# Kernel optimization log

Hardware: AMD Instinct MI355X
Metric: run time of the kernel (lower is better)

## Reference

```python
import jax, jax.numpy as jnp
import numpy as np

HEADS = 8
DIM_HEAD = 64


def setup_inputs() -> dict:
    key = jax.random.key(0)
    k1, k2, k3 = jax.random.split(key, 3)
    dim_in = 256
    hidden = HEADS * DIM_HEAD  # 512
    x = jax.random.normal(k1, (2, dim_in, 64, 64), dtype=jnp.float32)
    # 1x1 conv weights stored as [out_ch, in_ch]
    w_qkv = jax.random.normal(k2, (3 * hidden, dim_in), dtype=jnp.float32) * (1.0 / np.sqrt(dim_in))
    w_out = jax.random.normal(k3, (dim_in, hidden), dtype=jnp.float32) * (1.0 / np.sqrt(hidden))
    b_out = jnp.zeros((dim_in,), dtype=jnp.float32)
    return {"x": x, "w_qkv": w_qkv, "w_out": w_out, "b_out": b_out}


def reference(x, w_qkv, w_out, b_out):
    b, c, H, W = x.shape
    S = H * W
    scale = 1.0 / np.sqrt(DIM_HEAD)
    # 1x1 conv == per-pixel linear projection
    qkv = jnp.einsum('bcxy,oc->boxy', x, w_qkv)  # [b, 3*hidden, H, W]
    q, k, v = jnp.split(qkv, 3, axis=1)
    # 'b (h c) x y -> b h c (x y)'
    def to_heads(z):
        return z.reshape(b, HEADS, DIM_HEAD, S)
    q = to_heads(q) * scale
    k = to_heads(k)
    v = to_heads(v)
    sim = jnp.einsum('bhdi,bhdj->bhij', q, k)  # [b, h, S, S]
    sim = sim - jax.lax.stop_gradient(jnp.max(sim, axis=-1, keepdims=True))
    attn = jax.nn.softmax(sim, axis=-1)
    out = jnp.einsum('bhij,bhdj->bhid', attn, v)  # [b, h, S, d]
    # 'b h (x y) d -> b (h d) x y'
    out = out.transpose(0, 1, 3, 2).reshape(b, HEADS * DIM_HEAD, H, W)
    return jnp.einsum('bcxy,oc->boxy', out, w_out) + b_out[None, :, None, None]
```

## Files before the change

### kernel.cpp

```cpp
#include <hip/hip_runtime.h>
#include <cmath>

#define S_TOT 4096
#define CIN   256
#define HID   512
#define NHEAD 8
#define DIMH  64

typedef __attribute__((ext_vector_type(8))) short bf16x8;
typedef __attribute__((ext_vector_type(4))) float f32x4;
typedef __attribute__((ext_vector_type(16))) float f32x16;
typedef __attribute__((address_space(1))) const void gv_t;
typedef __attribute__((address_space(3))) void lv_t;

__device__ __forceinline__ ushort f2bf(float f) {
    union { float f; unsigned u; } v; v.f = f;
    unsigned r = (v.u + 0x7FFFu + ((v.u >> 16) & 1u)) >> 16;
    return (ushort)r;
}

__device__ __forceinline__ float bf2f(ushort u) {
    union { unsigned u; float f; } v; v.u = ((unsigned)u) << 16; return v.f;
}

__device__ __forceinline__ float exp2_fast(float x) {
    float r; asm("v_exp_f32 %0, %1" : "=v"(r) : "v"(x)); return r;
}

__device__ __forceinline__ unsigned cvt_pk_bf16(float lo, float hi) {
    unsigned r; asm("v_cvt_pk_bf16_f32 %0, %1, %2" : "=v"(r) : "v"(lo), "v"(hi)); return r;
}

#define QSCALE 0.18033688011112042f

__global__ __launch_bounds__(256)
void cast_f32_bf16(const float* __restrict__ in, ushort* __restrict__ out, long n) {
    long i = ((long)blockIdx.x * 256 + threadIdx.x) * 4;
    if (i < n) {
        float4 v = *(const float4*)&in[i];
        ushort4 p;
        p.x = f2bf(v.x); p.y = f2bf(v.y); p.z = f2bf(v.z); p.w = f2bf(v.w);
        *(ushort4*)&out[i] = p;
    }
}

__global__ __launch_bounds__(256)
void transpose_cast_x(const float* __restrict__ x, ushort* __restrict__ xt) {
    __shared__ float tb[64][65];
    const int t = threadIdx.x;
    const int s0 = blockIdx.x * 64, c0 = blockIdx.y * 64;
    const long xb = (long)blockIdx.z * CIN * S_TOT;
    #pragma unroll
    for (int i = 0; i < 16; ++i) {
        int idx = t + i * 256;
        int c = idx >> 6, s = idx & 63;
        tb[c][s] = x[xb + (long)(c0 + c) * S_TOT + s0 + s];
    }
    __syncthreads();
    const long ob = (long)blockIdx.z * S_TOT * CIN;
    const int s = t >> 2, cq = (t & 3) * 16;
    #pragma unroll
    for (int j = 0; j < 4; ++j) {
        ushort4 pk;
        pk.x = f2bf(tb[cq + j * 4 + 0][s]);
        pk.y = f2bf(tb[cq + j * 4 + 1][s]);
        pk.z = f2bf(tb[cq + j * 4 + 2][s]);
        pk.w = f2bf(tb[cq + j * 4 + 3][s]);
        *(ushort4*)&xt[ob + (long)(s0 + s) * CIN + c0 + cq + j * 4] = pk;
    }
}

template<int MODE>
__global__ __launch_bounds__(256)
void gemm_mfma_kernel(const ushort* __restrict__ Ag, const ushort* __restrict__ Bg,
                      void* __restrict__ outp, const float* __restrict__ bias,
                      int Kdim, long strideA, long strideB) {
    __shared__ __attribute__((aligned(16))) ushort Abuf[128 * 64];
    __shared__ __attribute__((aligned(16))) ushort Bbuf[128 * 64];
    const int t = threadIdx.x, lane = t & 63;
    const int l15 = lane & 15, g = lane >> 4;
    const int wid = t >> 6, wr = wid >> 1, wc = wid & 1;
    const int bz = blockIdx.z;
    const int am0 = blockIdx.y * 128, bn0 = blockIdx.x * 128;
    Ag += (long)bz * strideA;
    Bg += (long)bz * strideB;

    f32x4 acc[4][4];
    #pragma unroll
    for (int i = 0; i < 4; ++i)
        #pragma unroll
        for (int j = 0; j < 4; ++j)
            acc[i][j] = (f32x4){0.f, 0.f, 0.f, 0.f};

    for (int k0 = 0; k0 < Kdim; k0 += 64) {
        __syncthreads();
        #pragma unroll
        for (int i = 0; i < 4; ++i) {
            const int chunk = t + i * 256;
            const int row = chunk >> 3, sl = chunk & 7;
            const ushort* srcA = Ag + (long)(am0 + row) * Kdim + k0 + ((sl ^ (row & 7)) << 3);
            __builtin_amdgcn_global_load_lds((gv_t*)srcA,
                (lv_t*)((char*)Abuf + (i * 256 + (t & ~63)) * 16), 16, 0, 0);
            const ushort* srcB = Bg + (long)(bn0 + row) * Kdim + k0 + ((sl ^ (row & 7)) << 3);
            __builtin_amdgcn_global_load_lds((gv_t*)srcB,
                (lv_t*)((char*)Bbuf + (i * 256 + (t & ~63)) * 16), 16, 0, 0);
        }
        asm volatile("s_waitcnt vmcnt(0)" ::: "memory");
        __syncthreads();

        bf16x8 bfr[4][2];
        #pragma unroll
        for (int fn = 0; fn < 4; ++fn) {
            const int row = wc * 64 + fn * 16 + l15;
            #pragma unroll
            for (int hf = 0; hf < 2; ++hf)
                bfr[fn][hf] = *(const bf16x8*)((const char*)Bbuf + row * 128
                                + (((hf * 4 + g) ^ (row & 7)) << 4));
        }
        #pragma unroll
        for (int fm = 0; fm < 4; ++fm) {
            const int row = wr * 64 + fm * 16 + l15;
            const bf16x8 a0 = *(const bf16x8*)((const char*)Abuf + row * 128
                                + (((g) ^ (row & 7)) << 4));
            const bf16x8 a1 = *(const bf16x8*)((const char*)Abuf + row * 128
                                + (((4 + g) ^ (row & 7)) << 4));
            #pragma unroll
            for (int fn = 0; fn < 4; ++fn) {
                acc[fm][fn] = __builtin_amdgcn_mfma_f32_16x16x32_bf16(a0, bfr[fn][0], acc[fm][fn], 0, 0, 0);
                acc[fm][fn] = __builtin_amdgcn_mfma_f32_16x16x32_bf16(a1, bfr[fn][1], acc[fm][fn], 0, 0, 0);
            }
        }
    }

    #pragma unroll
    for (int fm = 0; fm < 4; ++fm)
        #pragma unroll
        for (int fn = 0; fn < 4; ++fn)
            #pragma unroll
            for (int r = 0; r < 4; ++r) {
                const int ar = am0 + wr * 64 + fm * 16 + g * 4 + r;
                const int bc = bn0 + wc * 64 + fn * 16 + l15;
                if (MODE == 0) {
                    const int which = bc >> 9, h = (bc >> 6) & 7, d = bc & 63;
                    const float scl = (which == 0) ? QSCALE : 1.0f;
                    ushort* O = (ushort*)outp;
                    O[(long)which * 4194304 + (((long)(bz * NHEAD + h)) * S_TOT + ar) * DIMH + d]
                        = f2bf(acc[fm][fn][r] * scl);
                } else if (MODE == 1) {
                    const int h = ar >> 6, d = ar & 63;
                    const int jm = bc & 15;
                    const int pjm = (jm & 3) | ((jm & 4) << 1) | ((jm & 8) >> 1);
                    const int pc = (bc & ~15) | pjm;
                    ushort* O = (ushort*)outp;
                    O[(((long)(bz * NHEAD + h)) * DIMH + d) * S_TOT + pc] = f2bf(acc[fm][fn][r]);
                } else {
                    float* O = (float*)outp;
                    O[((long)bz * CIN + ar) * S_TOT + bc] = acc[fm][fn][r] + bias[ar];
                }
            }
}

__global__ __launch_bounds__(256, 4)
void attn_mfma_kernel(const ushort* __restrict__ qg, const ushort* __restrict__ kg,
                      const ushort* __restrict__ vg, ushort* __restrict__ pout,
                      float2* __restrict__ mlout) {
    __shared__ __attribute__((aligned(16))) ushort kbuf[2][64 * 64];
    __shared__ __attribute__((aligned(16))) ushort vbuf[2][64 * 64];

    const int t = threadIdx.x;
    const int lane = t & 63, wid = t >> 6;
    const int l31 = lane & 31, h = lane >> 5;
    const int head = blockIdx.y;
    const int b = blockIdx.z >> 1, sp = blockIdx.z & 1;
    const int bh = b * NHEAD + head;
    const int qrow0 = blockIdx.x * 128 + wid * 32;
    const long kbase = (long)sp * (S_TOT / 2);

    const int sw_lo = (l31 ^ (l31 >> 3)) & 7;
    const int sw_hi = sw_lo ^ 4;

    const ushort* qp = qg + ((long)bh * S_TOT + qrow0 + l31) * DIMH + h * 8;
    bf16x8 qfr[4];
    #pragma unroll
    for (int ds = 0; ds < 4; ++ds) qfr[ds] = *(const bf16x8*)(qp + ds * 16);

    f32x16 oacc0 = {}, oacc1 = {};
    f32x16 bias16 = {};
    float nmr = 0.f, lrun = 0.f;

    const long kg_base = (long)bh * S_TOT * DIMH;
    const long vg_base = (long)bh * DIMH * S_TOT;
    const int sl = lane & 7, sr = lane >> 3;

    auto STAGE = [&](int buf, long key0) {
        #pragma unroll
        for (int c = 0; c < 2; ++c) {
            const int row = wid * 16 + c * 8 + sr;
            const int sz = (sl ^ sr ^ (wid * 2 + c)) & 7;
            char* kdst = (char*)(&kbuf[buf][0]) + wid * 2048 + c * 1024;
            char* vdst = (char*)(&vbuf[buf][0]) + wid * 2048 + c * 1024;
            const char* srcK = (const char*)(kg + kg_base + (key0 + row) * DIMH) + (sz << 4);
            __builtin_amdgcn_global_load_lds((gv_t*)srcK, (lv_t*)kdst, 16, 0, 0);
            const char* srcV = (const char*)(vg + vg_base + (long)row * S_TOT + key0) + (sz << 4);
            __builtin_amdgcn_global_load_lds((gv_t*)srcV, (lv_t*)vdst, 16, 0, 0);
        }
    };

    STAGE(0, kbase);
    asm volatile("s_waitcnt vmcnt(0)" ::: "memory");
    __syncthreads();

    const int NT = (S_TOT / 2) / 64;
    for (int kt0 = 0; kt0 < NT; ++kt0) {
        const int cur = kt0 & 1;
        if (kt0 + 1 < NT) STAGE(cur ^ 1, kbase + (long)(kt0 + 1) * 64);

        const char* kb_ = (const char*)(&kbuf[cur][0]);
        const char* vb_ = (const char*)(&vbuf[cur][0]);

        f32x16 s0, s1;
        __builtin_amdgcn_s_setprio(1);
        {
            const bf16x8 kf0 = *(const bf16x8*)(kb_ + l31 * 128 + ((h ^ sw_lo) << 4));
            const bf16x8 kf1 = *(const bf16x8*)(kb_ + 4096 + l31 * 128 + ((h ^ sw_hi) << 4));
            s0 = __builtin_amdgcn_mfma_f32_32x32x16_bf16(kf0, qfr[0], bias16, 0, 0, 0);
            s1 = __builtin_amdgcn_mfma_f32_32x32x16_bf16(kf1, qfr[0], bias16, 0, 0, 0);
        }
        #pragma unroll
        for (int ds = 1; ds < 4; ++ds) {
            const bf16x8 kf0 = *(const bf16x8*)(kb_ + l31 * 128 + (((2 * ds + h) ^ sw_lo) << 4));
            const bf16x8 kf1 = *(const bf16x8*)(kb_ + 4096 + l31 * 128 + (((2 * ds + h) ^ sw_hi) << 4));
            s0 = __builtin_amdgcn_mfma_f32_32x32x16_bf16(kf0, qfr[ds], s0, 0, 0, 0);
            s1 = __builtin_amdgcn_mfma_f32_32x32x16_bf16(kf1, qfr[ds], s1, 0, 0, 0);
        }
        __builtin_amdgcn_s_setprio(0);

        bf16x8 pf0, pf1, pf2, pf3;
        {
            float e[16];
            #pragma unroll
            for (int r = 0; r < 16; ++r) e[r] = exp2_fast(s0[r]);
            #pragma unroll
            for (int r = 0; r < 16; ++r) lrun += e[r];
            union { unsigned u[4]; bf16x8 v; } A_, B_;
            #pragma unroll
            for (int w = 0; w < 4; ++w) A_.u[w] = cvt_pk_bf16(e[2 * w], e[2 * w + 1]);
            #pragma unroll
            for (int w = 0; w < 4; ++w) B_.u[w] = cvt_pk_bf16(e[8 + 2 * w], e[9 + 2 * w]);
            pf0 = A_.v; pf1 = B_.v;
        }
        {
            float e[16];
            #pragma unroll
            for (int r = 0; r < 16; ++r) e[r] = exp2_fast(s1[r]);
            #pragma unroll
            for (int r = 0; r < 16; ++r) lrun += e[r];
            union { unsigned u[4]; bf16x8 v; } A_, B_;
            #pragma unroll
            for (int w = 0; w < 4; ++w) A_.u[w] = cvt_pk_bf16(e[2 * w], e[2 * w + 1]);
            #pragma unroll
            for (int w = 0; w < 4; ++w) B_.u[w] = cvt_pk_bf16(e[8 + 2 * w], e[9 + 2 * w]);
            pf2 = A_.v; pf3 = B_.v;
        }

        __builtin_amdgcn_s_setprio(1);
        {
            const bf16x8 vf00 = *(const bf16x8*)(vb_ + l31 * 128 + ((h ^ sw_lo) << 4));
            const bf16x8 vf01 = *(const bf16x8*)(vb_ + 4096 + l31 * 128 + ((h ^ sw_hi) << 4));
            oacc0 = __builtin_amdgcn_mfma_f32_32x32x16_bf16(pf0, vf00, oacc0, 0, 0, 0);
            oacc1 = __builtin_amdgcn_mfma_f32_32x32x16_bf16(pf0, vf01, oacc1, 0, 0, 0);
            const bf16x8 vf10 = *(const bf16x8*)(vb_ + l31 * 128 + (((2 + h) ^ sw_lo) << 4));
            const bf16x8 vf11 = *(const bf16x8*)(vb_ + 4096 + l31 * 128 + (((2 + h) ^ sw_hi) << 4));
            oacc0 = __builtin_amdgcn_mfma_f32_32x32x16_bf16(pf1, vf10, oacc0, 0, 0, 0);
            oacc1 = __builtin_amdgcn_mfma_f32_32x32x16_bf16(pf1, vf11, oacc1, 0, 0, 0);
            const bf16x8 vf20 = *(const bf16x8*)(vb_ + l31 * 128 + (((4 + h) ^ sw_lo) << 4));
            const bf16x8 vf21 = *(const bf16x8*)(vb_ + 4096 + l31 * 128 + (((4 + h) ^ sw_hi) << 4));
            oacc0 = __builtin_amdgcn_mfma_f32_32x32x16_bf16(pf2, vf20, oacc0, 0, 0, 0);
            oacc1 = __builtin_amdgcn_mfma_f32_32x32x16_bf16(pf2, vf21, oacc1, 0, 0, 0);
            const bf16x8 vf30 = *(const bf16x8*)(vb_ + l31 * 128 + (((6 + h) ^ sw_lo) << 4));
            const bf16x8 vf31 = *(const bf16x8*)(vb_ + 4096 + l31 * 128 + (((6 + h) ^ sw_hi) << 4));
            oacc0 = __builtin_amdgcn_mfma_f32_32x32x16_bf16(pf3, vf30, oacc0, 0, 0, 0);
            oacc1 = __builtin_amdgcn_mfma_f32_32x32x16_bf16(pf3, vf31, oacc1, 0, 0, 0);
        }
        __builtin_amdgcn_s_setprio(0);

        if (__any(lrun > 1.6777216e7f)) {
            const float sc = 5.9604644775390625e-8f;
            lrun *= sc;
            #pragma unroll
            for (int r = 0; r < 16; ++r) { oacc0[r] *= sc; oacc1[r] *= sc; }
            nmr -= 24.0f;
            #pragma unroll
            for (int r = 0; r < 16; ++r) bias16[r] = nmr;
        }

        asm volatile("s_waitcnt vmcnt(0)" ::: "memory");
        __syncthreads();
    }

    lrun += __shfl_xor(lrun, 32, 64);
    const long pbase = (((long)sp * 2 + b) * S_TOT) * HID;
    #pragma unroll
    for (int r = 0; r < 16; ++r) {
        const int q = (r & 3) + 8 * (r >> 2) + 4 * h;
        const long off = pbase + (long)(qrow0 + q) * HID + head * 64 + l31;
        pout[off]      = f2bf(oacc0[r]);
        pout[off + 32] = f2bf(oacc1[r]);
    }
    if (h == 0)
        mlout[((long)sp * 2 * NHEAD * S_TOT) + (long)bh * S_TOT + qrow0 + l31]
            = make_float2(-nmr, lrun);
}

__global__ __launch_bounds__(256)
void attn_merge_kernel(const ushort* __restrict__ part, const float2* __restrict__ ml,
                       ushort* __restrict__ aout) {
    const long i = (long)blockIdx.x * 256 + threadIdx.x;
    const int hd8 = (int)(i & 63);
    const long bq = i >> 6;
    const int q = (int)(bq & (S_TOT - 1)), b = (int)(bq >> 12);
    const int h = hd8 >> 3;
    const long mlst = (long)2 * NHEAD * S_TOT;
    const float2 ml0 = ml[(long)(b * NHEAD + h) * S_TOT + q];
    const float2 ml1 = ml[mlst + (long)(b * NHEAD + h) * S_TOT + q];
    const float m = fmaxf(ml0.x, ml1.x);
    const float w0 = exp2_fast(ml0.x - m), w1 = exp2_fast(ml1.x - m);
    const float inv = 1.0f / (w0 * ml0.y + w1 * ml1.y);
    const long phalf = (long)2 * S_TOT * HID;
    const long off = ((long)b * S_TOT + q) * HID + hd8 * 8;
    const bf16x8 p0 = *(const bf16x8*)&part[off];
    const bf16x8 p1 = *(const bf16x8*)&part[phalf + off];
    union { ushort u[8]; bf16x8 v; } o;
    #pragma unroll
    for (int j = 0; j < 8; ++j)
        o.u[j] = f2bf((w0 * bf2f((ushort)p0[j]) + w1 * bf2f((ushort)p1[j])) * inv);
    *(bf16x8*)&aout[off] = o.v;
}

extern "C" void kernel_launch(void* const* d_in, const int* in_sizes, int n_in,
                              void* d_out, int out_size, void* d_ws, size_t ws_size,
                              hipStream_t stream) {
    const float* x     = (const float*)d_in[0];
    const float* w_qkv = (const float*)d_in[1];
    const float* w_out = (const float*)d_in[2];
    const float* b_out = (const float*)d_in[3];
    float* out = (float*)d_out;

    const long PERQKV = (long)2 * NHEAD * S_TOT * DIMH;
    ushort* qws = (ushort*)d_ws;
    ushort* kws = qws + PERQKV;
    ushort* vws = kws + PERQKV;
    ushort* xt  = vws + PERQKV;
    ushort* wqb = xt + (long)2 * S_TOT * CIN;
    ushort* wob = wqb + (long)3 * HID * CIN;
    ushort* awb = wob + (long)CIN * HID;
    ushort* prt = awb + (long)2 * S_TOT * HID;
    float2* mlw = (float2*)(prt + (long)4 * S_TOT * HID);

    cast_f32_bf16<<<dim3((3 * HID * CIN / 4 + 255) / 256), 256, 0, stream>>>(
        w_qkv, wqb, (long)3 * HID * CIN);
    cast_f32_bf16<<<dim3((CIN * HID / 4 + 255) / 256), 256, 0, stream>>>(
        w_out, wob, (long)CIN * HID);
    transpose_cast_x<<<dim3(S_TOT / 64, CIN / 64, 2), 256, 0, stream>>>(x, xt);

    gemm_mfma_kernel<0><<<dim3(1024 / 128, S_TOT / 128, 2), 256, 0, stream>>>(
        xt, wqb, qws, nullptr, CIN, (long)S_TOT * CIN, 0L);
    gemm_mfma_kernel<1><<<dim3(S_TOT / 128, 512 / 128, 2), 256, 0, stream>>>(
        wqb + (long)1024 * CIN, xt, vws, nullptr, CIN, 0L, (long)S_TOT * CIN);

    attn_mfma_kernel<<<dim3(S_TOT / 128, NHEAD, 4), 256, 0, stream>>>(
        qws, kws, vws, prt, mlw);
    attn_merge_kernel<<<dim3((2 * S_TOT * 64) / 256), 256, 0, stream>>>(prt, mlw, awb);

    gemm_mfma_kernel<2><<<dim3(S_TOT / 128, CIN / 128, 2), 256, 0, stream>>>(
        wob, awb, out, b_out, HID, 0L, (long)S_TOT * HID);
}
```

Before: 127.6 us.

## Fuse prologue kernels, compute row sums via MFMA, split keys four ways

```diff
diff --git a/kernel.cpp b/kernel.cpp
--- a/kernel.cpp
+++ b/kernel.cpp
@@ -34,22 +34,26 @@
 #define QSCALE 0.18033688011112042f
 
 __global__ __launch_bounds__(256)
-void cast_f32_bf16(const float* __restrict__ in, ushort* __restrict__ out, long n) {
-    long i = ((long)blockIdx.x * 256 + threadIdx.x) * 4;
-    if (i < n) {
-        float4 v = *(const float4*)&in[i];
+void prologue_kernel(const float* __restrict__ w_qkv, const float* __restrict__ w_out,
+                     const float* __restrict__ x, ushort* __restrict__ wqb,
+                     ushort* __restrict__ wob, ushort* __restrict__ xt) {
+    __shared__ float tb[64][65];
+    const int bid = blockIdx.x, t = threadIdx.x;
+    if (bid < 512) {
+        const float* src = (bid < 384) ? w_qkv : w_out;
+        ushort* dst = (bid < 384) ? wqb : wob;
+        const long i = ((long)(bid < 384 ? bid : bid - 384) * 256 + t) * 4;
+        float4 v = *(const float4*)&src[i];
         ushort4 p;
         p.x = f2bf(v.x); p.y = f2bf(v.y); p.z = f2bf(v.z); p.w = f2bf(v.w);
-        *(ushort4*)&out[i] = p;
-    }
-}
-
-__global__ __launch_bounds__(256)
-void transpose_cast_x(const float* __restrict__ x, ushort* __restrict__ xt) {
-    __shared__ float tb[64][65];
-    const int t = threadIdx.x;
-    const int s0 = blockIdx.x * 64, c0 = blockIdx.y * 64;
-    const long xb = (long)blockIdx.z * CIN * S_TOT;
+        *(ushort4*)&dst[i] = p;
+        return;
+    }
+    const int xb_ = bid - 512;
+    const int sx = xb_ & 63, rest = xb_ >> 6;
+    const int cy = rest & 3, cz = rest >> 2;
+    const int s0 = sx * 64, c0 = cy * 64;
+    const long xb = (long)cz * CIN * S_TOT;
     #pragma unroll
     for (int i = 0; i < 16; ++i) {
         int idx = t + i * 256;
@@ -57,7 +61,7 @@
         tb[c][s] = x[xb + (long)(c0 + c) * S_TOT + s0 + s];
     }
     __syncthreads();
-    const long ob = (long)blockIdx.z * S_TOT * CIN;
+    const long ob = (long)cz * S_TOT * CIN;
     const int s = t >> 2, cq = (t & 3) * 16;
     #pragma unroll
     for (int j = 0; j < 4; ++j) {
@@ -160,6 +164,7 @@
             }
 }
 
+template<int NT>
 __global__ __launch_bounds__(256, 4)
 void attn_mfma_kernel(const ushort* __restrict__ qg, const ushort* __restrict__ kg,
                       const ushort* __restrict__ vg, ushort* __restrict__ pout,
@@ -171,10 +176,10 @@
     const int lane = t & 63, wid = t >> 6;
     const int l31 = lane & 31, h = lane >> 5;
     const int head = blockIdx.y;
-    const int b = blockIdx.z >> 1, sp = blockIdx.z & 1;
+    const int sp = blockIdx.z >> 1, b = blockIdx.z & 1;
     const int bh = b * NHEAD + head;
     const int qrow0 = blockIdx.x * 128 + wid * 32;
-    const long kbase = (long)sp * (S_TOT / 2);
+    const long kbase = (long)sp * (NT * 64);
 
     const int sw_lo = (l31 ^ (l31 >> 3)) & 7;
     const int sw_hi = sw_lo ^ 4;
@@ -184,9 +189,12 @@
     #pragma unroll
     for (int ds = 0; ds < 4; ++ds) qfr[ds] = *(const bf16x8*)(qp + ds * 16);
 
-    f32x16 oacc0 = {}, oacc1 = {};
+    const short ONE = (short)0x3F80;
+    const bf16x8 ones = {ONE, ONE, ONE, ONE, ONE, ONE, ONE, ONE};
+
+    f32x16 oacc0 = {}, oacc1 = {}, lacc = {};
     f32x16 bias16 = {};
-    float nmr = 0.f, lrun = 0.f;
+    float nmr = 0.f;
 
     const long kg_base = (long)bh * S_TOT * DIMH;
     const long vg_base = (long)bh * DIMH * S_TOT;
@@ -210,7 +218,6 @@
     asm volatile("s_waitcnt vmcnt(0)" ::: "memory");
     __syncthreads();
 
-    const int NT = (S_TOT / 2) / 64;
     for (int kt0 = 0; kt0 < NT; ++kt0) {
         const int cur = kt0 & 1;
         if (kt0 + 1 < NT) STAGE(cur ^ 1, kbase + (long)(kt0 + 1) * 64);
@@ -240,8 +247,6 @@
             float e[16];
             #pragma unroll
             for (int r = 0; r < 16; ++r) e[r] = exp2_fast(s0[r]);
-            #pragma unroll
-            for (int r = 0; r < 16; ++r) lrun += e[r];
             union { unsigned u[4]; bf16x8 v; } A_, B_;
             #pragma unroll
             for (int w = 0; w < 4; ++w) A_.u[w] = cvt_pk_bf16(e[2 * w], e[2 * w + 1]);
@@ -253,8 +258,6 @@
             float e[16];
             #pragma unroll
             for (int r = 0; r < 16; ++r) e[r] = exp2_fast(s1[r]);
-            #pragma unroll
-            for (int r = 0; r < 16; ++r) lrun += e[r];
             union { unsigned u[4]; bf16x8 v; } A_, B_;
             #pragma unroll
             for (int w = 0; w < 4; ++w) A_.u[w] = cvt_pk_bf16(e[2 * w], e[2 * w + 1]);
@@ -269,36 +272,45 @@
             const bf16x8 vf01 = *(const bf16x8*)(vb_ + 4096 + l31 * 128 + ((h ^ sw_hi) << 4));
             oacc0 = __builtin_amdgcn_mfma_f32_32x32x16_bf16(pf0, vf00, oacc0, 0, 0, 0);
             oacc1 = __builtin_amdgcn_mfma_f32_32x32x16_bf16(pf0, vf01, oacc1, 0, 0, 0);
+            lacc  = __builtin_amdgcn_mfma_f32_32x32x16_bf16(pf0, ones, lacc, 0, 0, 0);
             const bf16x8 vf10 = *(const bf16x8*)(vb_ + l31 * 128 + (((2 + h) ^ sw_lo) << 4));
             const bf16x8 vf11 = *(const bf16x8*)(vb_ + 4096 + l31 * 128 + (((2 + h) ^ sw_hi) << 4));
             oacc0 = __builtin_amdgcn_mfma_f32_32x32x16_bf16(pf1, vf10, oacc0, 0, 0, 0);
             oacc1 = __builtin_amdgcn_mfma_f32_32x32x16_bf16(pf1, vf11, oacc1, 0, 0, 0);
+            lacc  = __builtin_amdgcn_mfma_f32_32x32x16_bf16(pf1, ones, lacc, 0, 0, 0);
             const bf16x8 vf20 = *(const bf16x8*)(vb_ + l31 * 128 + (((4 + h) ^ sw_lo) << 4));
             const bf16x8 vf21 = *(const bf16x8*)(vb_ + 4096 + l31 * 128 + (((4 + h) ^ sw_hi) << 4));
             oacc0 = __builtin_amdgcn_mfma_f32_32x32x16_bf16(pf2, vf20, oacc0, 0, 0, 0);
             oacc1 = __builtin_amdgcn_mfma_f32_32x32x16_bf16(pf2, vf21, oacc1, 0, 0, 0);
+            lacc  = __builtin_amdgcn_mfma_f32_32x32x16_bf16(pf2, ones, lacc, 0, 0, 0);
             const bf16x8 vf30 = *(const bf16x8*)(vb_ + l31 * 128 + (((6 + h) ^ sw_lo) << 4));
             const bf16x8 vf31 = *(const bf16x8*)(vb_ + 4096 + l31 * 128 + (((6 + h) ^ sw_hi) << 4));
             oacc0 = __builtin_amdgcn_mfma_f32_32x32x16_bf16(pf3, vf30, oacc0, 0, 0, 0);
             oacc1 = __builtin_amdgcn_mfma_f32_32x32x16_bf16(pf3, vf31, oacc1, 0, 0, 0);
+            lacc  = __builtin_amdgcn_mfma_f32_32x32x16_bf16(pf3, ones, lacc, 0, 0, 0);
         }
         __builtin_amdgcn_s_setprio(0);
 
-        if (__any(lrun > 1.6777216e7f)) {
-            const float sc = 5.9604644775390625e-8f;
-            lrun *= sc;
-            #pragma unroll
-            for (int r = 0; r < 16; ++r) { oacc0[r] *= sc; oacc1[r] *= sc; }
-            nmr -= 24.0f;
-            #pragma unroll
-            for (int r = 0; r < 16; ++r) bias16[r] = nmr;
+        if ((kt0 & 7) == 7) {
+            float mx = lacc[0];
+            #pragma unroll
+            for (int r = 1; r < 16; ++r) mx = fmaxf(mx, lacc[r]);
+            if (__any(mx > 1.8446744e19f)) {
+                const float sc = 3.5527136788e-15f;
+                #pragma unroll
+                for (int r = 0; r < 16; ++r) {
+                    oacc0[r] *= sc; oacc1[r] *= sc; lacc[r] *= sc;
+                }
+                nmr -= 48.0f;
+                #pragma unroll
+                for (int r = 0; r < 16; ++r) bias16[r] = nmr;
+            }
         }
 
         asm volatile("s_waitcnt vmcnt(0)" ::: "memory");
         __syncthreads();
     }
 
-    lrun += __shfl_xor(lrun, 32, 64);
     const long pbase = (((long)sp * 2 + b) * S_TOT) * HID;
     #pragma unroll
     for (int r = 0; r < 16; ++r) {
@@ -307,11 +319,17 @@
         pout[off]      = f2bf(oacc0[r]);
         pout[off + 32] = f2bf(oacc1[r]);
     }
-    if (h == 0)
-        mlout[((long)sp * 2 * NHEAD * S_TOT) + (long)bh * S_TOT + qrow0 + l31]
-            = make_float2(-nmr, lrun);
-}
-
+    if (l31 == 0) {
+        float2* mlp = mlout + ((long)sp * 2 * NHEAD * S_TOT) + (long)bh * S_TOT + qrow0;
+        #pragma unroll
+        for (int r = 0; r < 16; ++r) {
+            const int q = (r & 3) + 8 * (r >> 2) + 4 * h;
+            mlp[q] = make_float2(-nmr, lacc[r]);
+        }
+    }
+}
+
+template<int SP>
 __global__ __launch_bounds__(256)
 void attn_merge_kernel(const ushort* __restrict__ part, const float2* __restrict__ ml,
                        ushort* __restrict__ aout) {
@@ -320,20 +338,35 @@
     const long bq = i >> 6;
     const int q = (int)(bq & (S_TOT - 1)), b = (int)(bq >> 12);
     const int h = hd8 >> 3;
-    const long mlst = (long)2 * NHEAD * S_TOT;
-    const float2 ml0 = ml[(long)(b * NHEAD + h) * S_TOT + q];
-    const float2 ml1 = ml[mlst + (long)(b * NHEAD + h) * S_TOT + q];
-    const float m = fmaxf(ml0.x, ml1.x);
-    const float w0 = exp2_fast(ml0.x - m), w1 = exp2_fast(ml1.x - m);
-    const float inv = 1.0f / (w0 * ml0.y + w1 * ml1.y);
-    const long phalf = (long)2 * S_TOT * HID;
+    const long mlsp = (long)2 * NHEAD * S_TOT;
+    const long mlidx = (long)(b * NHEAD + h) * S_TOT + q;
+    float2 mls[SP];
+    float m = -3e38f;
+    #pragma unroll
+    for (int sp = 0; sp < SP; ++sp) {
+        mls[sp] = ml[sp * mlsp + mlidx];
+        m = fmaxf(m, mls[sp].x);
+    }
+    float w[SP];
+    float wsum = 0.f;
+    #pragma unroll
+    for (int sp = 0; sp < SP; ++sp) {
+        w[sp] = exp2_fast(mls[sp].x - m);
+        wsum += w[sp] * mls[sp].y;
+    }
+    const float inv = 1.0f / wsum;
+    const long psp = (long)2 * S_TOT * HID;
     const long off = ((long)b * S_TOT + q) * HID + hd8 * 8;
-    const bf16x8 p0 = *(const bf16x8*)&part[off];
-    const bf16x8 p1 = *(const bf16x8*)&part[phalf + off];
+    float acc[8] = {};
+    #pragma unroll
+    for (int sp = 0; sp < SP; ++sp) {
+        const bf16x8 p = *(const bf16x8*)&part[sp * psp + off];
+        #pragma unroll
+        for (int j = 0; j < 8; ++j) acc[j] += w[sp] * bf2f((ushort)p[j]);
+    }
     union { ushort u[8]; bf16x8 v; } o;
     #pragma unroll
-    for (int j = 0; j < 8; ++j)
-        o.u[j] = f2bf((w0 * bf2f((ushort)p0[j]) + w1 * bf2f((ushort)p1[j])) * inv);
+    for (int j = 0; j < 8; ++j) o.u[j] = f2bf(acc[j] * inv);
     *(bf16x8*)&aout[off] = o.v;
 }
 
@@ -355,22 +388,29 @@
     ushort* wob = wqb + (long)3 * HID * CIN;
     ushort* awb = wob + (long)CIN * HID;
     ushort* prt = awb + (long)2 * S_TOT * HID;
-    float2* mlw = (float2*)(prt + (long)4 * S_TOT * HID);
-
-    cast_f32_bf16<<<dim3((3 * HID * CIN / 4 + 255) / 256), 256, 0, stream>>>(
-        w_qkv, wqb, (long)3 * HID * CIN);
-    cast_f32_bf16<<<dim3((CIN * HID / 4 + 255) / 256), 256, 0, stream>>>(
-        w_out, wob, (long)CIN * HID);
-    transpose_cast_x<<<dim3(S_TOT / 64, CIN / 64, 2), 256, 0, stream>>>(x, xt);
+
+    const long base_us = 3 * PERQKV + (long)2 * S_TOT * CIN + (long)3 * HID * CIN
+                       + (long)CIN * HID + (long)2 * S_TOT * HID;
+    const long need4 = (base_us + 4L * 2 * S_TOT * HID) * 2 + 4L * 2 * NHEAD * S_TOT * 8;
+    const int SP = (ws_size >= (size_t)need4) ? 4 : 2;
+    float2* mlw = (float2*)(prt + (long)SP * 2 * S_TOT * HID);
+
+    prologue_kernel<<<dim3(1024), 256, 0, stream>>>(w_qkv, w_out, x, wqb, wob, xt);
 
     gemm_mfma_kernel<0><<<dim3(1024 / 128, S_TOT / 128, 2), 256, 0, stream>>>(
         xt, wqb, qws, nullptr, CIN, (long)S_TOT * CIN, 0L);
     gemm_mfma_kernel<1><<<dim3(S_TOT / 128, 512 / 128, 2), 256, 0, stream>>>(
         wqb + (long)1024 * CIN, xt, vws, nullptr, CIN, 0L, (long)S_TOT * CIN);
 
-    attn_mfma_kernel<<<dim3(S_TOT / 128, NHEAD, 4), 256, 0, stream>>>(
-        qws, kws, vws, prt, mlw);
-    attn_merge_kernel<<<dim3((2 * S_TOT * 64) / 256), 256, 0, stream>>>(prt, mlw, awb);
+    if (SP == 4) {
+        attn_mfma_kernel<16><<<dim3(S_TOT / 128, NHEAD, 8), 256, 0, stream>>>(
+            qws, kws, vws, prt, mlw);
+        attn_merge_kernel<4><<<dim3((2 * S_TOT * 64) / 256), 256, 0, stream>>>(prt, mlw, awb);
+    } else {
+        attn_mfma_kernel<32><<<dim3(S_TOT / 128, NHEAD, 4), 256, 0, stream>>>(
+            qws, kws, vws, prt, mlw);
+        attn_merge_kernel<2><<<dim3((2 * S_TOT * 64) / 256), 256, 0, stream>>>(prt, mlw, awb);
+    }
 
     gemm_mfma_kernel<2><<<dim3(S_TOT / 128, CIN / 128, 2), 256, 0, stream>>>(
         wob, awb, out, b_out, HID, 0L, (long)S_TOT * HID);
```

Measured after the change: 193.7 us. +51.8%, slower.
